# Performance work log

Measured on AMD Instinct MI355X. Metric: run time of the kernel, lower is better.

## Reference

```python
import jax, jax.numpy as jnp
import numpy as np

N = 50000
E = 800000
NODE_C = 96
EDGE_C = 192
C1, C2, CMU = 125, 144, 163  # round(96+96*0.3), round(96+96*0.5), round(96+96*0.7)
DIVIDER = 10.0


def setup_inputs() -> dict:
    key = jax.random.key(0)
    ks = jax.random.split(key, 32)
    def w(k, i, o):
        return jax.random.normal(k, (i, o), jnp.float32) * (1.0 / np.sqrt(i))
    inp = {
        "x": jax.random.normal(ks[0], (N, NODE_C), jnp.float32),
        "edge_index": jax.random.randint(ks[1], (2, E), 0, N, dtype=jnp.int64),
        "eps_edge": jax.random.normal(ks[2], (N, CMU), jnp.float32),
        "eps_node": jax.random.normal(ks[3], (N, NODE_C), jnp.float32),
        "w1e": w(ks[4], NODE_C, C1), "b1e": jnp.zeros((C1,), jnp.float32),
        "w2e": w(ks[5], C1, C2),     "b2e": jnp.zeros((C2,), jnp.float32),
        "wme": w(ks[6], C2, CMU),    "bme": jnp.zeros((CMU,), jnp.float32),
        "wle": w(ks[7], C2, CMU),    "ble": jnp.zeros((CMU,), jnp.float32),
        "w4e": w(ks[8], CMU, EDGE_C),"b4e": jnp.zeros((EDGE_C,), jnp.float32),
        "w1n": w(ks[9], NODE_C, NODE_C), "b1n": jnp.zeros((NODE_C,), jnp.float32),
        "wmn": w(ks[10], NODE_C, NODE_C),"bmn": jnp.zeros((NODE_C,), jnp.float32),
        "wln": w(ks[11], NODE_C, NODE_C),"bln": jnp.zeros((NODE_C,), jnp.float32),
        "w5n": w(ks[12], NODE_C, NODE_C),"b5n": jnp.zeros((NODE_C,), jnp.float32),
    }
    return inp


def reference(x, edge_index, eps_edge, eps_node,
              w1e, b1e, w2e, b2e, wme, bme, wle, ble, w4e, b4e,
              w1n, b1n, wmn, bmn, wln, bln, w5n, b5n):
    row, col = edge_index[0], edge_index[1]
    n = x.shape[0]
    # GCN symmetric normalization with self-loops (deg counts incoming edges + 1)
    deg = jax.ops.segment_sum(jnp.ones(row.shape[0], x.dtype), col, num_segments=n) + 1.0
    dinv = deg ** -0.5
    coef = dinv[row] * dinv[col]          # [E]
    self_coef = (dinv * dinv)[:, None]    # [N,1] self-loop contribution

    def conv(h, W, b):
        hw = h @ W                                            # [N, out]
        agg = jax.ops.segment_sum(hw[row] * coef[:, None], col, num_segments=n)
        return agg + hw * self_coef + b

    # edge branch
    e = jax.nn.relu(conv(x, w1e, b1e))
    e = jax.nn.relu(conv(e, w2e, b2e))
    mu_e = conv(e, wme, bme)
    ls_e = conv(e, wle, ble)
    e = mu_e + eps_edge * jnp.exp(ls_e) / DIVIDER   # training-mode reparametrize
    edges = jax.nn.sigmoid(conv(e, w4e, b4e))

    # node branch
    nn_ = jax.nn.relu(conv(x, w1n, b1n))
    mu_n = conv(nn_, wmn, bmn)
    ls_n = conv(nn_, wln, bln)
    nn_ = mu_n + eps_node * jnp.exp(ls_n) / DIVIDER
    nodes = jax.nn.relu(conv(nn_, w5n, b5n))

    return edges, nodes
```

## Files before the change

kernel.cpp:

```cpp
#include <hip/hip_runtime.h>

typedef unsigned short u16;
typedef unsigned int u32;
typedef __bf16 bf16x8 __attribute__((ext_vector_type(8)));
typedef float f32x4 __attribute__((ext_vector_type(4)));

__device__ __forceinline__ u16 f2bf(float f) {
    u32 u = __float_as_uint(f);
    u32 r = (u + 0x7fffu + ((u >> 16) & 1u)) >> 16;
    return (u16)r;
}
__device__ __forceinline__ float bf2f(u16 v) { return __uint_as_float(((u32)v) << 16); }
__device__ __forceinline__ float bf_lo(u32 v) { return __uint_as_float(v << 16); }
__device__ __forceinline__ float bf_hi(u32 v) { return __uint_as_float(v & 0xffff0000u); }
__device__ __forceinline__ u32 pack2(float lo, float hi) {
    return (u32)f2bf(lo) | (((u32)f2bf(hi)) << 16);
}


__global__ void deg_kernel(const int* __restrict__ ei, int E, int* __restrict__ cnt) {
    int i = blockIdx.x * blockDim.x + threadIdx.x;
    if (i < E) atomicAdd(&cnt[ei[E + i]], 1);
}

__global__ void dinv_kernel(const int* __restrict__ cnt, float* __restrict__ dinv, int N) {
    int i = blockIdx.x * blockDim.x + threadIdx.x;
    if (i < N) dinv[i] = 1.0f / sqrtf((float)cnt[i] + 1.0f);
}


__global__ __launch_bounds__(256) void scan1_k(const int* __restrict__ cnt,
                                               int* __restrict__ offs,
                                               int* __restrict__ bsum, int N) {
    __shared__ int lds[256];
    int t = threadIdx.x;
    int idx0 = blockIdx.x * 1024 + t * 4;
    int v[4], s = 0;
#pragma unroll
    for (int k = 0; k < 4; k++) {
        int i = idx0 + k;
        v[k] = (i < N) ? cnt[i] : 0;
        s += v[k];
    }
    lds[t] = s;
    __syncthreads();
    for (int off = 1; off < 256; off <<= 1) {
        int u = 0;
        if (t >= off) u = lds[t - off];
        __syncthreads();
        lds[t] += u;
        __syncthreads();
    }
    int run = lds[t] - s;
#pragma unroll
    for (int k = 0; k < 4; k++) {
        int i = idx0 + k;
        if (i < N) offs[i] = run;
        run += v[k];
    }
    if (t == 255) bsum[blockIdx.x] = lds[255];
}

__global__ __launch_bounds__(256) void scan2_k(int* __restrict__ bsum, int* __restrict__ boff,
                                               int nb, int* __restrict__ totp) {
    __shared__ int lds[256];
    int t = threadIdx.x;
    int s = (t < nb) ? bsum[t] : 0;
    lds[t] = s;
    __syncthreads();
    for (int off = 1; off < 256; off <<= 1) {
        int u = 0;
        if (t >= off) u = lds[t - off];
        __syncthreads();
        lds[t] += u;
        __syncthreads();
    }
    if (t < nb) boff[t] = lds[t] - s;
    if (t == 255) *totp = lds[255];
}

__global__ void scan3_k(int* __restrict__ offs, int* __restrict__ cursor,
                        const int* __restrict__ boff, int N) {
    int i = blockIdx.x * blockDim.x + threadIdx.x;
    if (i < N) {
        int v = offs[i] + boff[i >> 10];
        offs[i] = v;
        cursor[i] = v;
    }
}

__global__ void fill_kernel(const int* __restrict__ ei, int E,
                            const float* __restrict__ dinv, int* __restrict__ cursor,
                            int2* __restrict__ csr) {
    int i = blockIdx.x * blockDim.x + threadIdx.x;
    if (i < E) {
        int r = ei[i];
        int c = ei[E + i];
        int pos = atomicAdd(&cursor[c], 1);
        csr[pos] = make_int2(r, __float_as_int(dinv[r]));
    }
}


__global__ void cvt_f2bf_k(const float* __restrict__ src, u16* __restrict__ dst, int npairs) {
    u32* d = (u32*)dst;
    for (int i = blockIdx.x * blockDim.x + threadIdx.x; i < npairs;
         i += blockDim.x * gridDim.x) {
        float lo = src[2 * i], hi = src[2 * i + 1];
        d[i] = pack2(lo, hi);
    }
}


struct PackArgs {
    const float* W[9];
    const float* B[9];
    int Kin[9], Nout[9], KS[9], NT[9], wOff[9], bOff[9];
};

__global__ void pack_weights(PackArgs pa, u16* __restrict__ wpack, float* __restrict__ bpack) {
    int L = blockIdx.y;
    int KS = pa.KS[L], NT = pa.NT[L], Kin = pa.Kin[L], Nout = pa.Nout[L];
    int wtot = KS * NT * 512;
    int btot = NT * 16;
    const float* W = pa.W[L];
    const float* Bb = pa.B[L];
    u16* wp = wpack + pa.wOff[L];
    float* bp = bpack + pa.bOff[L];
    for (int idx = blockIdx.x * blockDim.x + threadIdx.x; idx < wtot + btot;
         idx += blockDim.x * gridDim.x) {
        if (idx < wtot) {
            int j = idx & 7;
            int lane = (idx >> 3) & 63;
            int pos = idx >> 9;
            int jt = pos % NT;
            int ks = pos / NT;
            int k = ks * 32 + ((lane >> 4) & 3) * 8 + j;
            int n = jt * 16 + (lane & 15);
            u16 v = 0;
            if (k < Kin && n < Nout) v = f2bf(W[k * Nout + n]);
            wp[idx] = v;
        } else {
            int n = idx - wtot;
            float v = 0.f;
            if (n < Nout) v = Bb[n];
            bp[n] = v;
        }
    }
}


template <int C2>
__global__ __launch_bounds__(256) void propagate_k(const u16* __restrict__ h,
                                                   u16* __restrict__ out,
                                                   const float* __restrict__ dinv,
                                                   const int* __restrict__ offs,
                                                   const int2* __restrict__ csr, int N) {
    constexpr int Cp = C2 * 2;
    const int lane = threadIdx.x & 63;
    int wid = (blockIdx.x * blockDim.x + threadIdx.x) >> 6;
    int nw = (gridDim.x * blockDim.x) >> 6;
    constexpr bool HAS1 = (C2 > 64);
    const bool a0 = lane < (C2 < 64 ? C2 : 64);
    const bool a1 = HAS1 && (lane < C2 - 64);
    const int c0 = lane, c1 = lane + 64;
    for (int n = wid; n < N; n += nw) {
        float dn = dinv[n];
        int beg = offs[n], end = offs[n + 1];
        float x0 = 0.f, y0 = 0.f, x1 = 0.f, y1 = 0.f;
        {
            const u32* hp = (const u32*)(h + (size_t)n * Cp);
            if (a0) { u32 v = hp[c0]; x0 = dn * bf_lo(v); y0 = dn * bf_hi(v); }
            if (a1) { u32 v = hp[c1]; x1 = dn * bf_lo(v); y1 = dn * bf_hi(v); }
        }
        int e = beg;
        for (; e + 3 < end; e += 4) {
            int2 c_0 = csr[e], c_1 = csr[e + 1], c_2 = csr[e + 2], c_3 = csr[e + 3];
            float w0 = __int_as_float(c_0.y), w1 = __int_as_float(c_1.y);
            float w2 = __int_as_float(c_2.y), w3 = __int_as_float(c_3.y);
            const u32* p0 = (const u32*)(h + (size_t)c_0.x * Cp);
            const u32* p1 = (const u32*)(h + (size_t)c_1.x * Cp);
            const u32* p2 = (const u32*)(h + (size_t)c_2.x * Cp);
            const u32* p3 = (const u32*)(h + (size_t)c_3.x * Cp);
            if (a0) {
                u32 u0 = p0[c0], u1 = p1[c0], u2 = p2[c0], u3 = p3[c0];
                x0 = fmaf(w0, bf_lo(u0), x0); y0 = fmaf(w0, bf_hi(u0), y0);
                x0 = fmaf(w1, bf_lo(u1), x0); y0 = fmaf(w1, bf_hi(u1), y0);
                x0 = fmaf(w2, bf_lo(u2), x0); y0 = fmaf(w2, bf_hi(u2), y0);
                x0 = fmaf(w3, bf_lo(u3), x0); y0 = fmaf(w3, bf_hi(u3), y0);
            }
            if (a1) {
                u32 u0 = p0[c1], u1 = p1[c1], u2 = p2[c1], u3 = p3[c1];
                x1 = fmaf(w0, bf_lo(u0), x1); y1 = fmaf(w0, bf_hi(u0), y1);
                x1 = fmaf(w1, bf_lo(u1), x1); y1 = fmaf(w1, bf_hi(u1), y1);
                x1 = fmaf(w2, bf_lo(u2), x1); y1 = fmaf(w2, bf_hi(u2), y1);
                x1 = fmaf(w3, bf_lo(u3), x1); y1 = fmaf(w3, bf_hi(u3), y1);
            }
        }
        for (; e < end; e++) {
            int2 ce = csr[e];
            float w0 = __int_as_float(ce.y);
            const u32* p0 = (const u32*)(h + (size_t)ce.x * Cp);
            if (a0) { u32 u = p0[c0]; x0 = fmaf(w0, bf_lo(u), x0); y0 = fmaf(w0, bf_hi(u), y0); }
            if (a1) { u32 u = p0[c1]; x1 = fmaf(w0, bf_lo(u), x1); y1 = fmaf(w0, bf_hi(u), y1); }
        }
        u32* op = (u32*)(out + (size_t)n * Cp);
        if (a0) op[c0] = pack2(dn * x0, dn * y0);
        if (a1) op[c1] = pack2(dn * x1, dn * y1);
    }
}


template <int KS, int NTtot, int NTH>
__device__ __forceinline__ void gemm_body(const u16* A, const u16* Bp, int jBase,
                                          f32x4* acc, int m0, int M, int lane) {
    constexpr int Kp = KS * 32;
    int row = m0 + (lane & 15);
    if (row >= M) row = M - 1;
    const u16* aptr = A + (size_t)row * Kp + ((lane >> 4) * 8);
    const u16* bptr = Bp + lane * 8;
#pragma unroll
    for (int j = 0; j < NTH; j++) acc[j] = (f32x4){0.f, 0.f, 0.f, 0.f};
#pragma unroll
    for (int ks = 0; ks < KS; ks++) {
        bf16x8 af = *(const bf16x8*)(aptr + ks * 32);
#pragma unroll
        for (int j = 0; j < NTH; j++) {
            bf16x8 bf = *(const bf16x8*)(bptr + (ks * NTtot + jBase + j) * 512);
            acc[j] = __builtin_amdgcn_mfma_f32_16x16x32_bf16(af, bf, acc[j], 0, 0, 0);
        }
    }
}

template <int KS, int NTtot, int NTH, int OP, int OUTF>
__global__ __launch_bounds__(256) void gemm_k(const u16* __restrict__ A,
                                              const u16* __restrict__ Bp,
                                              const float* __restrict__ bias,
                                              void* __restrict__ Cv, int M, int ldc) {
    const int lane = threadIdx.x & 63;
    const int wave = threadIdx.x >> 6;
    const int jBase = blockIdx.y * NTH;
    int m0 = (blockIdx.x * 4 + wave) * 16;
    if (m0 >= M) return;
    f32x4 acc[NTH];
    gemm_body<KS, NTtot, NTH>(A, Bp, jBase, acc, m0, M, lane);
    int mrow = m0 + (lane >> 4) * 4;
#pragma unroll
    for (int j = 0; j < NTH; j++) {
        int n = (jBase + j) * 16 + (lane & 15);
        float b = bias[n];
#pragma unroll
        for (int r = 0; r < 4; r++) {
            int m = mrow + r;
            if (m < M) {
                float v = acc[j][r] + b;
                if (OP == 1) v = fmaxf(v, 0.f);
                if (OP == 2) v = 1.f / (1.f + expf(-v));
                if (OUTF) ((float*)Cv)[(size_t)m * ldc + n] = v;
                else ((u16*)Cv)[(size_t)m * ldc + n] = f2bf(v);
            }
        }
    }
}

template <int KS, int NT1, int NT2>
__global__ __launch_bounds__(256) void gemm_dual_relu_k(const u16* __restrict__ A,
                                                        const u16* __restrict__ Bp1,
                                                        const float* __restrict__ bias1,
                                                        u16* __restrict__ C1o, int ld1,
                                                        const u16* __restrict__ Bp2,
                                                        const float* __restrict__ bias2,
                                                        u16* __restrict__ C2o, int ld2, int M) {
    const int lane = threadIdx.x & 63;
    const int wave = threadIdx.x >> 6;
    int m0 = (blockIdx.x * 4 + wave) * 16;
    if (m0 >= M) return;
    int mrow = m0 + (lane >> 4) * 4;
    if (blockIdx.y == 0) {
        f32x4 acc[NT1];
        gemm_body<KS, NT1, NT1>(A, Bp1, 0, acc, m0, M, lane);
#pragma unroll
        for (int j = 0; j < NT1; j++) {
            int n = j * 16 + (lane & 15);
            float b = bias1[n];
#pragma unroll
            for (int r = 0; r < 4; r++) {
                int m = mrow + r;
                if (m < M) C1o[(size_t)m * ld1 + n] = f2bf(fmaxf(acc[j][r] + b, 0.f));
            }
        }
    } else {
        f32x4 acc[NT2];
        gemm_body<KS, NT2, NT2>(A, Bp2, 0, acc, m0, M, lane);
#pragma unroll
        for (int j = 0; j < NT2; j++) {
            int n = j * 16 + (lane & 15);
            float b = bias2[n];
#pragma unroll
            for (int r = 0; r < 4; r++) {
                int m = mrow + r;
                if (m < M) C2o[(size_t)m * ld2 + n] = f2bf(fmaxf(acc[j][r] + b, 0.f));
            }
        }
    }
}

template <int KS, int NTtot, int NTH, int CLIM>
__global__ __launch_bounds__(256) void gemm_reparam_k(const u16* __restrict__ A,
                                                      const u16* __restrict__ BpM,
                                                      const float* __restrict__ biasM,
                                                      const u16* __restrict__ BpL,
                                                      const float* __restrict__ biasL,
                                                      const u16* __restrict__ epsb,
                                                      u16* __restrict__ out, int ldc, int M) {
    const int lane = threadIdx.x & 63;
    const int wave = threadIdx.x >> 6;
    const int jBase = blockIdx.y * NTH;
    int m0 = (blockIdx.x * 4 + wave) * 16;
    if (m0 >= M) return;
    int mrow = m0 + (lane >> 4) * 4;
    float epsv[NTH * 4];
#pragma unroll
    for (int j = 0; j < NTH; j++) {
        int n = (jBase + j) * 16 + (lane & 15);
#pragma unroll
        for (int r = 0; r < 4; r++) {
            int m = mrow + r;
            if (m >= M) m = M - 1;
            epsv[j * 4 + r] = (n < CLIM) ? bf2f(epsb[(size_t)m * CLIM + n]) : 0.f;
        }
    }
    constexpr int Kp = KS * 32;
    int row = m0 + (lane & 15);
    if (row >= M) row = M - 1;
    const u16* aptr = A + (size_t)row * Kp + ((lane >> 4) * 8);
    f32x4 accM[NTH], accL[NTH];
#pragma unroll
    for (int j = 0; j < NTH; j++) {
        accM[j] = (f32x4){0.f, 0.f, 0.f, 0.f};
        accL[j] = (f32x4){0.f, 0.f, 0.f, 0.f};
    }
#pragma unroll
    for (int ks = 0; ks < KS; ks++) {
        bf16x8 af = *(const bf16x8*)(aptr + ks * 32);
#pragma unroll
        for (int j = 0; j < NTH; j++) {
            bf16x8 bm = *(const bf16x8*)(BpM + lane * 8 + (ks * NTtot + jBase + j) * 512);
            accM[j] = __builtin_amdgcn_mfma_f32_16x16x32_bf16(af, bm, accM[j], 0, 0, 0);
            bf16x8 bl = *(const bf16x8*)(BpL + lane * 8 + (ks * NTtot + jBase + j) * 512);
            accL[j] = __builtin_amdgcn_mfma_f32_16x16x32_bf16(af, bl, accL[j], 0, 0, 0);
        }
    }
#pragma unroll
    for (int j = 0; j < NTH; j++) {
        int n = (jBase + j) * 16 + (lane & 15);
        float bm = biasM[n];
        float bl = biasL[n];
#pragma unroll
        for (int r = 0; r < 4; r++) {
            int m = mrow + r;
            if (m < M) {
                float v = 0.f;
                if (n < CLIM)
                    v = (accM[j][r] + bm) + epsv[j * 4 + r] * expf(accL[j][r] + bl) * 0.1f;
                out[(size_t)m * ldc + n] = f2bf(v);
            }
        }
    }
}


extern "C" void kernel_launch(void* const* d_in, const int* in_sizes, int n_in,
                              void* d_out, int out_size, void* d_ws, size_t ws_size,
                              hipStream_t stream) {
    const float* x = (const float*)d_in[0];
    const int* ei = (const int*)d_in[1];
    const float* eps_e = (const float*)d_in[2];
    const float* eps_n = (const float*)d_in[3];
    int N = in_sizes[0] / 96;
    int E = in_sizes[1] / 2;

    char* p = (char*)d_ws;
    auto alloc = [&](size_t bytes) -> char* {
        char* r = p;
        p += (bytes + 255) & ~(size_t)255;
        return r;
    };
    int* cnt = (int*)alloc((size_t)N * 4);
    float* dinv = (float*)alloc((size_t)N * 4);
    int* offs = (int*)alloc((size_t)(N + 1) * 4);
    int* cursor = (int*)alloc((size_t)N * 4);
    int* bsum = (int*)alloc(256 * 4);
    int* boff = (int*)alloc(256 * 4);
    int2* csr = (int2*)alloc((size_t)E * 8);
    u16* wpack = (u16*)alloc(167936 * 2);
    float* bpack = (float*)alloc(1248 * 4);
    size_t bufBytes = (size_t)N * 192 * 2;
    u16* bufA = (u16*)alloc(bufBytes);
    u16* bufB = (u16*)alloc(bufBytes);
    u16* bufC = (u16*)alloc(bufBytes);
    u16* bufD = (u16*)alloc(bufBytes);
    u16* epsEb = (u16*)alloc((size_t)N * 163 * 2);
    u16* epsNb = (u16*)alloc((size_t)N * 96 * 2);

    hipMemsetAsync(cnt, 0, (size_t)N * 4, stream);
    int gE = (E + 255) / 256, gN = (N + 255) / 256;
    deg_kernel<<<gE, 256, 0, stream>>>(ei, E, cnt);
    dinv_kernel<<<gN, 256, 0, stream>>>(cnt, dinv, N);
    int nb = (N + 1023) / 1024;
    scan1_k<<<nb, 256, 0, stream>>>(cnt, offs, bsum, N);
    scan2_k<<<1, 256, 0, stream>>>(bsum, boff, nb, offs + N);
    scan3_k<<<gN, 256, 0, stream>>>(offs, cursor, boff, N);
    fill_kernel<<<gE, 256, 0, stream>>>(ei, E, dinv, cursor, csr);

    static const int wi[9] = {4, 6, 8, 10, 12, 14, 16, 18, 20};
    static const int bi[9] = {5, 7, 9, 11, 13, 15, 17, 19, 21};
    static const int Kin[9] = {96, 125, 144, 144, 163, 96, 96, 96, 96};
    static const int Nout[9] = {125, 144, 163, 163, 192, 96, 96, 96, 96};
    static const int KSa[9] = {3, 4, 5, 5, 6, 3, 3, 3, 3};
    static const int NTa[9] = {8, 10, 12, 12, 12, 6, 6, 6, 6};
    static const int wOff[9] = {0, 12288, 32768, 63488, 94208, 131072, 140288, 149504, 158720};
    static const int bOff[9] = {0, 128, 288, 480, 672, 864, 960, 1056, 1152};
    PackArgs pa;
    for (int i = 0; i < 9; i++) {
        pa.W[i] = (const float*)d_in[wi[i]];
        pa.B[i] = (const float*)d_in[bi[i]];
        pa.Kin[i] = Kin[i]; pa.Nout[i] = Nout[i];
        pa.KS[i] = KSa[i];  pa.NT[i] = NTa[i];
        pa.wOff[i] = wOff[i]; pa.bOff[i] = bOff[i];
    }
    pack_weights<<<dim3(32, 9), 256, 0, stream>>>(pa, wpack, bpack);

    const int gp = 2048;
    const int gg = (N + 63) / 64;

    cvt_f2bf_k<<<2048, 256, 0, stream>>>(x, bufD, N * 48);
    propagate_k<48><<<gp, 256, 0, stream>>>(bufD, bufA, dinv, offs, csr, N);
    gemm_dual_relu_k<3, 8, 6><<<dim3(gg, 2), 256, 0, stream>>>(
        bufA, wpack + 0, bpack + 0, bufC, 128, wpack + 131072, bpack + 864, bufB, 96, N);
    propagate_k<64><<<gp, 256, 0, stream>>>(bufC, bufA, dinv, offs, csr, N);
    gemm_k<4, 10, 5, 1, 0><<<dim3(gg, 2), 256, 0, stream>>>(bufA, wpack + 12288, bpack + 128,
                                                            bufC, N, 160);
    propagate_k<80><<<gp, 256, 0, stream>>>(bufC, bufA, dinv, offs, csr, N);
    cvt_f2bf_k<<<2048, 256, 0, stream>>>(eps_e, epsEb, N * 163 / 2);
    gemm_reparam_k<5, 12, 6, 163><<<dim3(gg, 2), 256, 0, stream>>>(
        bufA, wpack + 32768, bpack + 288, wpack + 63488, bpack + 480, epsEb, bufC, 192, N);
    propagate_k<96><<<gp, 256, 0, stream>>>(bufC, bufD, dinv, offs, csr, N);
    gemm_k<6, 12, 6, 2, 1><<<dim3(gg, 2), 256, 0, stream>>>(bufD, wpack + 94208, bpack + 672,
                                                            (float*)d_out, N, 192);
    propagate_k<48><<<gp, 256, 0, stream>>>(bufB, bufA, dinv, offs, csr, N);
    cvt_f2bf_k<<<2048, 256, 0, stream>>>(eps_n, epsNb, N * 48);
    gemm_reparam_k<3, 6, 3, 96><<<dim3(gg, 2), 256, 0, stream>>>(
        bufA, wpack + 140288, bpack + 960, wpack + 149504, bpack + 1056, epsNb, bufC, 96, N);
    propagate_k<48><<<gp, 256, 0, stream>>>(bufC, bufA, dinv, offs, csr, N);
    gemm_k<3, 6, 3, 1, 1><<<dim3(gg, 2), 256, 0, stream>>>(bufA, wpack + 158720, bpack + 1152,
                                                           (float*)d_out + (size_t)N * 192, N, 96);
}
```

Baseline: 671.5 us.

## Unroll gather loop to 8, propagate fp32 input directly, split GEMM column tiles

The propagate gather loop is unrolled from 4 to 8 edges so more independent loads are in flight per wave. A new fp32 propagate kernel reads x directly and drops the separate bf16 conversion pass. The GEMMs preload A fragments into registers and split output columns across more grid-y blocks, giving more, smaller blocks per GEMM. The trade-off is higher register pressure in the gather and repeated A-row loads across the extra column blocks.

```diff
diff --git a/kernel.cpp b/kernel.cpp
--- a/kernel.cpp
+++ b/kernel.cpp
@@ -174,39 +174,93 @@
             if (a1) { u32 v = hp[c1]; x1 = dn * bf_lo(v); y1 = dn * bf_hi(v); }
         }
         int e = beg;
-        for (; e + 3 < end; e += 4) {
-            int2 c_0 = csr[e], c_1 = csr[e + 1], c_2 = csr[e + 2], c_3 = csr[e + 3];
-            float w0 = __int_as_float(c_0.y), w1 = __int_as_float(c_1.y);
-            float w2 = __int_as_float(c_2.y), w3 = __int_as_float(c_3.y);
-            const u32* p0 = (const u32*)(h + (size_t)c_0.x * Cp);
-            const u32* p1 = (const u32*)(h + (size_t)c_1.x * Cp);
-            const u32* p2 = (const u32*)(h + (size_t)c_2.x * Cp);
-            const u32* p3 = (const u32*)(h + (size_t)c_3.x * Cp);
+        for (; e + 7 < end; e += 8) {
+            int2 ce[8];
+#pragma unroll
+            for (int k = 0; k < 8; k++) ce[k] = csr[e + k];
+            const u32* ps[8];
+#pragma unroll
+            for (int k = 0; k < 8; k++) ps[k] = (const u32*)(h + (size_t)ce[k].x * Cp);
             if (a0) {
-                u32 u0 = p0[c0], u1 = p1[c0], u2 = p2[c0], u3 = p3[c0];
-                x0 = fmaf(w0, bf_lo(u0), x0); y0 = fmaf(w0, bf_hi(u0), y0);
-                x0 = fmaf(w1, bf_lo(u1), x0); y0 = fmaf(w1, bf_hi(u1), y0);
-                x0 = fmaf(w2, bf_lo(u2), x0); y0 = fmaf(w2, bf_hi(u2), y0);
-                x0 = fmaf(w3, bf_lo(u3), x0); y0 = fmaf(w3, bf_hi(u3), y0);
+                u32 uu[8];
+#pragma unroll
+                for (int k = 0; k < 8; k++) uu[k] = ps[k][c0];
+#pragma unroll
+                for (int k = 0; k < 8; k++) {
+                    float w = __int_as_float(ce[k].y);
+                    x0 = fmaf(w, bf_lo(uu[k]), x0); y0 = fmaf(w, bf_hi(uu[k]), y0);
+                }
             }
             if (a1) {
-                u32 u0 = p0[c1], u1 = p1[c1], u2 = p2[c1], u3 = p3[c1];
-                x1 = fmaf(w0, bf_lo(u0), x1); y1 = fmaf(w0, bf_hi(u0), y1);
-                x1 = fmaf(w1, bf_lo(u1), x1); y1 = fmaf(w1, bf_hi(u1), y1);
-                x1 = fmaf(w2, bf_lo(u2), x1); y1 = fmaf(w2, bf_hi(u2), y1);
-                x1 = fmaf(w3, bf_lo(u3), x1); y1 = fmaf(w3, bf_hi(u3), y1);
+                u32 uu[8];
+#pragma unroll
+                for (int k = 0; k < 8; k++) uu[k] = ps[k][c1];
+#pragma unroll
+                for (int k = 0; k < 8; k++) {
+                    float w = __int_as_float(ce[k].y);
+                    x1 = fmaf(w, bf_lo(uu[k]), x1); y1 = fmaf(w, bf_hi(uu[k]), y1);
+                }
             }
         }
         for (; e < end; e++) {
-            int2 ce = csr[e];
-            float w0 = __int_as_float(ce.y);
-            const u32* p0 = (const u32*)(h + (size_t)ce.x * Cp);
+            int2 cek = csr[e];
+            float w0 = __int_as_float(cek.y);
+            const u32* p0 = (const u32*)(h + (size_t)cek.x * Cp);
             if (a0) { u32 u = p0[c0]; x0 = fmaf(w0, bf_lo(u), x0); y0 = fmaf(w0, bf_hi(u), y0); }
             if (a1) { u32 u = p0[c1]; x1 = fmaf(w0, bf_lo(u), x1); y1 = fmaf(w0, bf_hi(u), y1); }
         }
         u32* op = (u32*)(out + (size_t)n * Cp);
         if (a0) op[c0] = pack2(dn * x0, dn * y0);
         if (a1) op[c1] = pack2(dn * x1, dn * y1);
+    }
+}
+
+template <int C2>
+__global__ __launch_bounds__(256) void propagate_f32_k(const float* __restrict__ h,
+                                                       u16* __restrict__ out,
+                                                       const float* __restrict__ dinv,
+                                                       const int* __restrict__ offs,
+                                                       const int2* __restrict__ csr, int N) {
+    constexpr int Cp = C2 * 2;
+    const int lane = threadIdx.x & 63;
+    int wid = (blockIdx.x * blockDim.x + threadIdx.x) >> 6;
+    int nw = (gridDim.x * blockDim.x) >> 6;
+    const bool a0 = lane < C2;
+    const int c0 = lane;
+    for (int n = wid; n < N; n += nw) {
+        float dn = dinv[n];
+        int beg = offs[n], end = offs[n + 1];
+        float x0 = 0.f, y0 = 0.f;
+        if (a0) {
+            float2 v = ((const float2*)(h + (size_t)n * Cp))[c0];
+            x0 = dn * v.x; y0 = dn * v.y;
+        }
+        int e = beg;
+        for (; e + 7 < end; e += 8) {
+            int2 ce[8];
+#pragma unroll
+            for (int k = 0; k < 8; k++) ce[k] = csr[e + k];
+            if (a0) {
+                float2 vv[8];
+#pragma unroll
+                for (int k = 0; k < 8; k++)
+                    vv[k] = ((const float2*)(h + (size_t)ce[k].x * Cp))[c0];
+#pragma unroll
+                for (int k = 0; k < 8; k++) {
+                    float w = __int_as_float(ce[k].y);
+                    x0 = fmaf(w, vv[k].x, x0); y0 = fmaf(w, vv[k].y, y0);
+                }
+            }
+        }
+        for (; e < end; e++) {
+            int2 cek = csr[e];
+            float w0 = __int_as_float(cek.y);
+            if (a0) {
+                float2 v = ((const float2*)(h + (size_t)cek.x * Cp))[c0];
+                x0 = fmaf(w0, v.x, x0); y0 = fmaf(w0, v.y, y0);
+            }
+        }
+        if (a0) ((u32*)(out + (size_t)n * Cp))[c0] = pack2(dn * x0, dn * y0);
     }
 }
 
@@ -219,15 +273,17 @@
     if (row >= M) row = M - 1;
     const u16* aptr = A + (size_t)row * Kp + ((lane >> 4) * 8);
     const u16* bptr = Bp + lane * 8;
+    bf16x8 afr[KS];
+#pragma unroll
+    for (int ks = 0; ks < KS; ks++) afr[ks] = *(const bf16x8*)(aptr + ks * 32);
 #pragma unroll
     for (int j = 0; j < NTH; j++) acc[j] = (f32x4){0.f, 0.f, 0.f, 0.f};
 #pragma unroll
     for (int ks = 0; ks < KS; ks++) {
-        bf16x8 af = *(const bf16x8*)(aptr + ks * 32);
 #pragma unroll
         for (int j = 0; j < NTH; j++) {
             bf16x8 bf = *(const bf16x8*)(bptr + (ks * NTtot + jBase + j) * 512);
-            acc[j] = __builtin_amdgcn_mfma_f32_16x16x32_bf16(af, bf, acc[j], 0, 0, 0);
+            acc[j] = __builtin_amdgcn_mfma_f32_16x16x32_bf16(afr[ks], bf, acc[j], 0, 0, 0);
         }
     }
 }
@@ -263,7 +319,7 @@
     }
 }
 
-template <int KS, int NT1, int NT2>
+template <int KS, int NT1, int NTH1, int Y1, int NT2, int NTH2>
 __global__ __launch_bounds__(256) void gemm_dual_relu_k(const u16* __restrict__ A,
                                                         const u16* __restrict__ Bp1,
                                                         const float* __restrict__ bias1,
@@ -276,12 +332,13 @@
     int m0 = (blockIdx.x * 4 + wave) * 16;
     if (m0 >= M) return;
     int mrow = m0 + (lane >> 4) * 4;
-    if (blockIdx.y == 0) {
-        f32x4 acc[NT1];
-        gemm_body<KS, NT1, NT1>(A, Bp1, 0, acc, m0, M, lane);
-#pragma unroll
-        for (int j = 0; j < NT1; j++) {
-            int n = j * 16 + (lane & 15);
+    if ((int)blockIdx.y < Y1) {
+        int jBase = blockIdx.y * NTH1;
+        f32x4 acc[NTH1];
+        gemm_body<KS, NT1, NTH1>(A, Bp1, jBase, acc, m0, M, lane);
+#pragma unroll
+        for (int j = 0; j < NTH1; j++) {
+            int n = (jBase + j) * 16 + (lane & 15);
             float b = bias1[n];
 #pragma unroll
             for (int r = 0; r < 4; r++) {
@@ -290,11 +347,12 @@
             }
         }
     } else {
-        f32x4 acc[NT2];
-        gemm_body<KS, NT2, NT2>(A, Bp2, 0, acc, m0, M, lane);
-#pragma unroll
-        for (int j = 0; j < NT2; j++) {
-            int n = j * 16 + (lane & 15);
+        int jBase = (blockIdx.y - Y1) * NTH2;
+        f32x4 acc[NTH2];
+        gemm_body<KS, NT2, NTH2>(A, Bp2, jBase, acc, m0, M, lane);
+#pragma unroll
+        for (int j = 0; j < NTH2; j++) {
+            int n = (jBase + j) * 16 + (lane & 15);
             float b = bias2[n];
 #pragma unroll
             for (int r = 0; r < 4; r++) {
@@ -319,6 +377,13 @@
     int m0 = (blockIdx.x * 4 + wave) * 16;
     if (m0 >= M) return;
     int mrow = m0 + (lane >> 4) * 4;
+    constexpr int Kp = KS * 32;
+    int row = m0 + (lane & 15);
+    if (row >= M) row = M - 1;
+    const u16* aptr = A + (size_t)row * Kp + ((lane >> 4) * 8);
+    bf16x8 afr[KS];
+#pragma unroll
+    for (int ks = 0; ks < KS; ks++) afr[ks] = *(const bf16x8*)(aptr + ks * 32);
     float epsv[NTH * 4];
 #pragma unroll
     for (int j = 0; j < NTH; j++) {
@@ -330,10 +395,6 @@
             epsv[j * 4 + r] = (n < CLIM) ? bf2f(epsb[(size_t)m * CLIM + n]) : 0.f;
         }
     }
-    constexpr int Kp = KS * 32;
-    int row = m0 + (lane & 15);
-    if (row >= M) row = M - 1;
-    const u16* aptr = A + (size_t)row * Kp + ((lane >> 4) * 8);
     f32x4 accM[NTH], accL[NTH];
 #pragma unroll
     for (int j = 0; j < NTH; j++) {
@@ -342,13 +403,12 @@
     }
 #pragma unroll
     for (int ks = 0; ks < KS; ks++) {
-        bf16x8 af = *(const bf16x8*)(aptr + ks * 32);
 #pragma unroll
         for (int j = 0; j < NTH; j++) {
             bf16x8 bm = *(const bf16x8*)(BpM + lane * 8 + (ks * NTtot + jBase + j) * 512);
-            accM[j] = __builtin_amdgcn_mfma_f32_16x16x32_bf16(af, bm, accM[j], 0, 0, 0);
+            accM[j] = __builtin_amdgcn_mfma_f32_16x16x32_bf16(afr[ks], bm, accM[j], 0, 0, 0);
             bf16x8 bl = *(const bf16x8*)(BpL + lane * 8 + (ks * NTtot + jBase + j) * 512);
-            accL[j] = __builtin_amdgcn_mfma_f32_16x16x32_bf16(af, bl, accL[j], 0, 0, 0);
+            accL[j] = __builtin_amdgcn_mfma_f32_16x16x32_bf16(afr[ks], bl, accL[j], 0, 0, 0);
         }
     }
 #pragma unroll
@@ -434,25 +494,24 @@
     const int gp = 2048;
     const int gg = (N + 63) / 64;
 
-    cvt_f2bf_k<<<2048, 256, 0, stream>>>(x, bufD, N * 48);
-    propagate_k<48><<<gp, 256, 0, stream>>>(bufD, bufA, dinv, offs, csr, N);
-    gemm_dual_relu_k<3, 8, 6><<<dim3(gg, 2), 256, 0, stream>>>(
+    propagate_f32_k<48><<<gp, 256, 0, stream>>>(x, bufA, dinv, offs, csr, N);
+    gemm_dual_relu_k<3, 8, 4, 2, 6, 3><<<dim3(gg, 4), 256, 0, stream>>>(
         bufA, wpack + 0, bpack + 0, bufC, 128, wpack + 131072, bpack + 864, bufB, 96, N);
     propagate_k<64><<<gp, 256, 0, stream>>>(bufC, bufA, dinv, offs, csr, N);
-    gemm_k<4, 10, 5, 1, 0><<<dim3(gg, 2), 256, 0, stream>>>(bufA, wpack + 12288, bpack + 128,
+    gemm_k<4, 10, 2, 1, 0><<<dim3(gg, 5), 256, 0, stream>>>(bufA, wpack + 12288, bpack + 128,
                                                             bufC, N, 160);
     propagate_k<80><<<gp, 256, 0, stream>>>(bufC, bufA, dinv, offs, csr, N);
     cvt_f2bf_k<<<2048, 256, 0, stream>>>(eps_e, epsEb, N * 163 / 2);
-    gemm_reparam_k<5, 12, 6, 163><<<dim3(gg, 2), 256, 0, stream>>>(
+    gemm_reparam_k<5, 12, 3, 163><<<dim3(gg, 4), 256, 0, stream>>>(
         bufA, wpack + 32768, bpack + 288, wpack + 63488, bpack + 480, epsEb, bufC, 192, N);
     propagate_k<96><<<gp, 256, 0, stream>>>(bufC, bufD, dinv, offs, csr, N);
-    gemm_k<6, 12, 6, 2, 1><<<dim3(gg, 2), 256, 0, stream>>>(bufD, wpack + 94208, bpack + 672,
+    gemm_k<6, 12, 3, 2, 1><<<dim3(gg, 4), 256, 0, stream>>>(bufD, wpack + 94208, bpack + 672,
                                                             (float*)d_out, N, 192);
     propagate_k<48><<<gp, 256, 0, stream>>>(bufB, bufA, dinv, offs, csr, N);
     cvt_f2bf_k<<<2048, 256, 0, stream>>>(eps_n, epsNb, N * 48);
-    gemm_reparam_k<3, 6, 3, 96><<<dim3(gg, 2), 256, 0, stream>>>(
+    gemm_reparam_k<3, 6, 2, 96><<<dim3(gg, 3), 256, 0, stream>>>(
         bufA, wpack + 140288, bpack + 960, wpack + 149504, bpack + 1056, epsNb, bufC, 96, N);
     propagate_k<48><<<gp, 256, 0, stream>>>(bufC, bufA, dinv, offs, csr, N);
-    gemm_k<3, 6, 3, 1, 1><<<dim3(gg, 2), 256, 0, stream>>>(bufA, wpack + 158720, bpack + 1152,
+    gemm_k<3, 6, 2, 1, 1><<<dim3(gg, 3), 256, 0, stream>>>(bufA, wpack + 158720, bpack + 1152,
                                                            (float*)d_out + (size_t)N * 192, N, 96);
 }
```

Result: no change. 678.2 us (+1.0%).
